# Kernel optimization log

Hardware: AMD Instinct MI355X
Metric: run time of the kernel (lower is better)

Reference implementation:

```python
import jax, jax.numpy as jnp
import numpy as np

BATCH, SEQ, HIDDEN = 2, 4096, 4096
HEADS, HEAD_DIM, BLOCK = 32, 128, 256
LAYER_IDX, N_LAYERS = 1, 32
EPS = 1e-5


def setup_inputs() -> dict:
    key = jax.random.key(0)
    ks = jax.random.split(key, 5)
    s = 0.02
    return {
        "hidden_states": jax.random.normal(ks[0], (BATCH, SEQ, HIDDEN), jnp.float32),
        "qkv_w": jax.random.normal(ks[1], (3 * HEADS * HEAD_DIM, HIDDEN), jnp.float32) * s,
        "out_w": jax.random.normal(ks[2], (HIDDEN, HEADS * HEAD_DIM), jnp.float32) * s,
        "gate_w": jax.random.normal(ks[3], (HEADS * HEAD_DIM, HIDDEN), jnp.float32) * s,
        "norm_w": jnp.ones((HEADS * HEAD_DIM,), jnp.float32),
    }


def _decays():
    # slope_rate: (h,1,1)
    base = 1.0 / 2.0 ** (8.0 / HEADS)
    exponent = jnp.arange(HEADS, dtype=jnp.float32) + 1.0
    factor = 1.0 - LAYER_IDX / (N_LAYERS - 1 + 1e-5) + 1e-5
    slope = (base ** exponent * factor)[:, None, None]
    r = jnp.arange(BLOCK, dtype=jnp.float32) + 1.0
    q_decay = jnp.exp(-slope * r[:, None])                 # (h, block, 1)
    k_decay = jnp.exp(-slope * (BLOCK - r)[:, None])       # (h, block, 1)
    diff = r[:, None] - r[None, :]                         # (block, block): i - j
    diag = slope[None] * diff[None, None]                  # (1, h, block, block)
    diag = jnp.where(diag >= 0, -diag, -jnp.inf)
    diag_decay = jnp.exp(diag)                             # causal intra-block decay
    block_decay = jnp.exp(-slope * BLOCK)                  # (h,1,1)
    return q_decay, k_decay, diag_decay, block_decay


def reference(hidden_states, qkv_w, out_w, gate_w, norm_w):
    b, s, _ = hidden_states.shape
    h, d, bs = HEADS, HEAD_DIM, BLOCK
    nb = s // bs
    q_decay, k_decay, diag_decay, block_decay = _decays()

    # qkv projection + silu, split per-head into q,k,v
    qkv = jax.nn.silu(hidden_states @ qkv_w.T)             # (b,s,3hd)
    qkv = qkv.reshape(b, s, h, 3, d)
    q = jnp.moveaxis(qkv[:, :, :, 0], 2, 1)                # (b,h,s,d)
    k = jnp.moveaxis(qkv[:, :, :, 1], 2, 1)
    v = jnp.moveaxis(qkv[:, :, :, 2], 2, 1)

    # split sequence into blocks, scan leading axis = block index
    def to_blocks(x):
        return jnp.moveaxis(x.reshape(b, h, nb, bs, d), 2, 0)  # (nb,b,h,bs,d)

    qb, kb, vb = to_blocks(q), to_blocks(k), to_blocks(v)

    def step(kv, blk):
        cq, ck, cv = blk
        # intra-block quadratic attention with causal decay
        scores = jnp.einsum('bhnd,bhmd->bhnm', cq, ck) * diag_decay
        intra = jnp.einsum('bhnm,bhmd->bhnd', scores, cv)
        # inter-block via decayed recurrent state kv: (b,h,d,d)
        inter = jnp.einsum('bhnd,bhde->bhne', cq * q_decay, kv)
        kv_next = kv * block_decay + jnp.einsum('bhnd,bhne->bhde', ck * k_decay, cv)
        return kv_next, intra + inter

    kv0 = jnp.zeros((b, h, d, d), hidden_states.dtype)
    _, out_blocks = jax.lax.scan(step, kv0, (qb, kb, vb))  # (nb,b,h,bs,d)

    attn = jnp.moveaxis(out_blocks, 0, 2)                  # (b,h,nb,bs,d)
    attn = attn.reshape(b, h, s, d).transpose(0, 2, 1, 3).reshape(b, s, h * d)

    # RMSNorm (fp32 accumulation, as MixtralRMSNorm)
    xf = attn.astype(jnp.float32)
    xf = xf * jax.lax.rsqrt(jnp.mean(xf * xf, axis=-1, keepdims=True) + EPS)
    normed = norm_w * xf.astype(attn.dtype)

    gate = jax.nn.sigmoid(hidden_states @ gate_w.T)
    return (gate * normed) @ out_w.T
```

## Files before the change

### kernel.cpp

```cpp
#include <hip/hip_runtime.h>

typedef unsigned short u16;
typedef __attribute__((ext_vector_type(4))) float f32x4;
typedef __attribute__((ext_vector_type(8))) __bf16 bf16x8;

#define SEQ   4096
#define HID   4096
#define HID3  12288

__device__ __forceinline__ float bf2f(u16 u){
  union { unsigned int i; float f; } v; v.i = ((unsigned int)u) << 16; return v.f;
}
__device__ __forceinline__ u16 f2bf(float f){
  union { float f; unsigned int i; } v; v.f = f;
  unsigned int r = (v.i + 0x7FFFu + ((v.i >> 16) & 1u)) >> 16;
  return (u16)r;
}
__device__ __forceinline__ float slope_of(int h){
  const float factor = 1.0f - 1.0f/(31.0f + 1e-5f) + 1e-5f;
  return exp2f(-0.25f * (float)(h + 1)) * factor;
}
__device__ __forceinline__ bf16x8 ld_bf8(const u16* p){
  return __builtin_bit_cast(bf16x8, *(const uint4*)p);
}
__device__ __forceinline__ void gload_lds16(const u16* g, u16* l){
  __builtin_amdgcn_global_load_lds((const __attribute__((address_space(1))) void*)g,
                                   (__attribute__((address_space(3))) void*)l, 16, 0, 0);
}

#define CVT_B0 33554432L
#define CVT_B1 83886080L
#define CVT_B2 100663296L
#define CVT_B3 117440512L
__global__ __launch_bounds__(256) void cvt4_kernel(const float* __restrict__ s0,
                                                   const float* __restrict__ s1,
                                                   const float* __restrict__ s2,
                                                   const float* __restrict__ s3,
                                                   u16* __restrict__ dst){
  long i = ((long)blockIdx.x * 256 + threadIdx.x) * 4;
  long stride = (long)gridDim.x * 1024;
  for (; i < CVT_B3; i += stride){
    const float* src;
    long off;
    if (i < CVT_B0){ src = s0; off = i; }
    else if (i < CVT_B1){ src = s1; off = i - CVT_B0; }
    else if (i < CVT_B2){ src = s2; off = i - CVT_B1; }
    else { src = s3; off = i - CVT_B2; }
    float4 v = *(const float4*)(src + off);
    ushort4 o;
    o.x = f2bf(v.x); o.y = f2bf(v.y); o.z = f2bf(v.z); o.w = f2bf(v.w);
    *(ushort4*)(dst + i) = o;
  }
}

template<int EPI>
__global__ __launch_bounds__(512) void gemm256(
    const u16* __restrict__ A, const u16* __restrict__ B, void* __restrict__ C,
    const u16* __restrict__ Aux, int M, int N, int K)
{
  __shared__ u16 ring[5][16384];
  const int t = threadIdx.x;
  const int w = t >> 6, l = t & 63, lr = l & 15, lk = l >> 4;
  const int mw = w >> 2, nw = w & 3;
  const int nbn = N >> 8;
  int nwg = gridDim.x;
  int bid = blockIdx.x;
  int bswz = (bid & 7) * (nwg >> 3) + (bid >> 3);
  int bm = bswz / nbn, bn = bswz % nbn;
  const u16* Abase = A + (long)(bm * 256) * K;
  const u16* Bbase = B + (long)(bn * 256) * K;
  const int NT = K >> 6;

  int sr[2], sku[2];
#pragma unroll
  for (int i = 0; i < 2; ++i){
    int dr = i * 64 + (t >> 3);
    int ul = (t & 7) ^ (dr & 7);
    sr[i]  = 2 * dr + (ul >> 2);
    sku[i] = ul & 3;
  }
  int offA[8], offB[4];
#pragma unroll
  for (int fn = 0; fn < 8; ++fn){
    int row = mw * 128 + fn * 16 + lr;
    offA[fn] = (row >> 1) * 64 + (((((row & 1) << 2) + lk) ^ ((row >> 1) & 7)) << 3);
  }
#pragma unroll
  for (int fe = 0; fe < 4; ++fe){
    int row = nw * 64 + fe * 16 + lr;
    offB[fe] = (row >> 1) * 64 + (((((row & 1) << 2) + lk) ^ ((row >> 1) & 7)) << 3);
  }

  auto stageA = [&](int kt, int c, int slot, int i){
    gload_lds16(Abase + (long)sr[i] * K + kt * 64 + c * 32 + sku[i] * 8,
                &ring[slot][i * 4096 + w * 512]);
  };
  auto stageB = [&](int kt, int c, int slot, int i){
    gload_lds16(Bbase + (long)sr[i] * K + kt * 64 + c * 32 + sku[i] * 8,
                &ring[slot][8192 + i * 4096 + w * 512]);
  };

  f32x4 acc[8][4] = {};

  stageA(0,0,0,0); stageA(0,0,0,1); stageB(0,0,0,0); stageB(0,0,0,1);
  stageA(0,1,1,0); stageA(0,1,1,1); stageB(0,1,1,0); stageB(0,1,1,1);
  if (1 < NT){ stageA(1,0,2,0); stageA(1,0,2,1); stageB(1,0,2,0); stageB(1,0,2,1); }
  asm volatile("s_waitcnt vmcnt(4)" ::: "memory");
  __builtin_amdgcn_s_barrier();

  int sa = 0;
  for (int p = 0; p < NT; ++p){
    int sb = sa + 1; if (sb >= 5) sb -= 5;
    int sx = sa + 3; if (sx >= 5) sx -= 5;
    int sy = sa + 4; if (sy >= 5) sy -= 5;
    const u16* Aa = &ring[sa][0];
    const u16* Ab = &ring[sb][0];
    const u16* Ba = &ring[sa][8192];
    const u16* Bb = &ring[sb][8192];
    bf16x8 bh0[4], bh1[4], afc0[8], afc1[8];

#pragma unroll
    for (int fe = 0; fe < 4; ++fe) bh0[fe] = ld_bf8(Ba + offB[fe]);
#pragma unroll
    for (int fn = 0; fn < 4; ++fn) afc0[fn] = ld_bf8(Aa + offA[fn]);
#pragma unroll
    for (int fn = 4; fn < 8; ++fn) afc0[fn] = ld_bf8(Aa + offA[fn]);
    if (p + 1 < NT){ stageA(p+1, 1, sx, 0); stageA(p+1, 1, sx, 1); }
    asm volatile("s_waitcnt lgkmcnt(4)" ::: "memory");
    __builtin_amdgcn_sched_barrier(0);
    __builtin_amdgcn_s_setprio(1);
#pragma unroll
    for (int fn = 0; fn < 4; ++fn)
#pragma unroll
      for (int fe = 0; fe < 4; ++fe)
        acc[fn][fe] = __builtin_amdgcn_mfma_f32_16x16x32_bf16(afc0[fn], bh0[fe], acc[fn][fe], 0, 0, 0);
    __builtin_amdgcn_s_setprio(0);

#pragma unroll
    for (int fe = 0; fe < 4; ++fe) bh1[fe] = ld_bf8(Bb + offB[fe]);
#pragma unroll
    for (int fn = 0; fn < 4; ++fn) afc1[fn] = ld_bf8(Ab + offA[fn]);
    if (p + 1 < NT){ stageB(p+1, 1, sx, 0); stageB(p+1, 1, sx, 1); }
    asm volatile("s_waitcnt lgkmcnt(8)" ::: "memory");
    __builtin_amdgcn_sched_barrier(0);
    __builtin_amdgcn_s_setprio(1);
#pragma unroll
    for (int fn = 4; fn < 8; ++fn)
#pragma unroll
      for (int fe = 0; fe < 4; ++fe)
        acc[fn][fe] = __builtin_amdgcn_mfma_f32_16x16x32_bf16(afc0[fn], bh0[fe], acc[fn][fe], 0, 0, 0);
    __builtin_amdgcn_s_setprio(0);

#pragma unroll
    for (int fn = 4; fn < 8; ++fn) afc1[fn] = ld_bf8(Ab + offA[fn]);
    if (p + 2 < NT){ stageA(p+2, 0, sy, 0); stageA(p+2, 0, sy, 1); }
    asm volatile("s_waitcnt lgkmcnt(4)" ::: "memory");
    __builtin_amdgcn_sched_barrier(0);
    __builtin_amdgcn_s_setprio(1);
#pragma unroll
    for (int fn = 0; fn < 4; ++fn)
#pragma unroll
      for (int fe = 0; fe < 4; ++fe)
        acc[fn][fe] = __builtin_amdgcn_mfma_f32_16x16x32_bf16(afc1[fn], bh1[fe], acc[fn][fe], 0, 0, 0);
    __builtin_amdgcn_s_setprio(0);

    if (p + 2 < NT){ stageB(p+2, 0, sy, 0); stageB(p+2, 0, sy, 1); }
    asm volatile("s_waitcnt lgkmcnt(0)" ::: "memory");
    __builtin_amdgcn_sched_barrier(0);
    __builtin_amdgcn_s_setprio(1);
#pragma unroll
    for (int fn = 4; fn < 8; ++fn)
#pragma unroll
      for (int fe = 0; fe < 4; ++fe)
        acc[fn][fe] = __builtin_amdgcn_mfma_f32_16x16x32_bf16(afc1[fn], bh1[fe], acc[fn][fe], 0, 0, 0);
    __builtin_amdgcn_s_setprio(0);

    if (p + 2 < NT) asm volatile("s_waitcnt vmcnt(4)" ::: "memory");
    else            asm volatile("s_waitcnt vmcnt(0)" ::: "memory");
    __builtin_amdgcn_s_barrier();
    sa += 2; if (sa >= 5) sa -= 5;
  }

  long crow = (long)bm * 256 + mw * 128 + lk * 4;
  long ccol = (long)bn * 256 + nw * 64 + lr;
#pragma unroll
  for (int fn = 0; fn < 8; ++fn)
#pragma unroll
    for (int fe = 0; fe < 4; ++fe)
#pragma unroll
      for (int reg = 0; reg < 4; ++reg){
        long row = crow + fn * 16 + reg;
        long col = ccol + fe * 16;
        float x = acc[fn][fe][reg];
        if (EPI == 0){
          ((u16*)C)[row * N + col] = f2bf(x / (1.0f + __expf(-x)));
        } else if (EPI == 1){
          float g = 1.0f / (1.0f + __expf(-x));
          ((u16*)C)[row * N + col] = f2bf(g * bf2f(Aux[row * N + col]));
        } else {
          ((float*)C)[row * N + col] = x;
        }
      }
}

__global__ __launch_bounds__(256) void attn_contrib(
    const u16* __restrict__ qkv, float* __restrict__ ct)
{
  __shared__ u16 VT[128 * 258];
  __shared__ u16 KT[128 * 258];
  int wg = blockIdx.x;
  int bh = wg >> 4, blk = wg & 15;
  int b = bh >> 5, h = bh & 31;
  int t = threadIdx.x;
  float slope = slope_of(h);
  const u16* kg = qkv + ((long)(b * SEQ + blk * 256)) * HID3 + h * 384 + 128;
  const u16* vg = kg + 128;
#pragma unroll
  for (int i = 0; i < 16; ++i){
    int chunk = t + i * 256;
    int row = chunk >> 4, c8 = (chunk & 15) << 3;
    float kd = __expf(-slope * (float)(255 - row));
    uint4 kk = *(const uint4*)&kg[(long)row * HID3 + c8];
    uint4 vv = *(const uint4*)&vg[(long)row * HID3 + c8];
    const u16* ks = (const u16*)&kk;
    const u16* vs = (const u16*)&vv;
#pragma unroll
    for (int x = 0; x < 8; ++x){
      KT[(c8 + x) * 258 + row] = f2bf(bf2f(ks[x]) * kd);
      VT[(c8 + x) * 258 + row] = vs[x];
    }
  }
  __syncthreads();
  int w = t >> 6, l = t & 63, lr = l & 15, lk = l >> 4;
  int we = (w >> 1) * 64, wd = (w & 1) * 64;
  f32x4 acc[4][4] = {};
  for (int nc = 0; nc < 8; ++nc){
    bf16x8 va[4], kb[4];
#pragma unroll
    for (int f = 0; f < 4; ++f) va[f] = ld_bf8(&VT[(we + f * 16 + lr) * 258 + nc * 32 + lk * 8]);
#pragma unroll
    for (int f = 0; f < 4; ++f) kb[f] = ld_bf8(&KT[(wd + f * 16 + lr) * 258 + nc * 32 + lk * 8]);
#pragma unroll
    for (int fe = 0; fe < 4; ++fe)
#pragma unroll
      for (int fd = 0; fd < 4; ++fd)
        acc[fe][fd] = __builtin_amdgcn_mfma_f32_16x16x32_bf16(va[fe], kb[fd], acc[fe][fd], 0, 0, 0);
  }
  float* out = ct + (long)wg * 16384;
#pragma unroll
  for (int fe = 0; fe < 4; ++fe)
#pragma unroll
    for (int fd = 0; fd < 4; ++fd)
#pragma unroll
      for (int reg = 0; reg < 4; ++reg){
        int e = we + fe * 16 + lk * 4 + reg;
        int d = wd + fd * 16 + lr;
        out[e * 128 + d] = acc[fe][fd][reg];
      }
}

__global__ __launch_bounds__(256) void attn_scan(const float* __restrict__ ct,
                                                 u16* __restrict__ stTb)
{
  int g = blockIdx.x;
  int bh = g >> 2, sl = g & 3;
  int t = threadIdx.x;
  float bdec = __expf(-slope_of(bh & 31) * 256.0f);
  float cur[16];
#pragma unroll
  for (int i = 0; i < 16; ++i) cur[i] = 0.f;
  const float* base = ct + (long)bh * 16 * 16384 + sl * 4096;
  u16* ob = stTb + (long)bh * 16 * 16384 + sl * 4096;
  for (int blkI = 0; blkI < 16; ++blkI){
    const float* p = base + (long)blkI * 16384;
    u16* o = ob + (long)blkI * 16384;
#pragma unroll
    for (int i = 0; i < 16; ++i){
      o[t + i * 256] = f2bf(cur[i]);
      cur[i] = cur[i] * bdec + p[t + i * 256];
    }
  }
}

__global__ __launch_bounds__(512) void attn_mfma(
    const u16* __restrict__ qkv, const u16* __restrict__ stTb, u16* __restrict__ attn)
{
  __shared__ u16 Ks[256 * 130];
  __shared__ u16 VTs[128 * 258];
  __shared__ u16 Ps[4][64 * 34];
  int wg = blockIdx.x;
  int bh = wg >> 4, blk = wg & 15;
  int b = bh >> 5, h = bh & 31;
  int t = threadIdx.x;
  int w = t >> 6, l = t & 63, lr = l & 15, lk = l >> 4;
  int r = w >> 1, c = w & 1;
  float slope = slope_of(h);
  const u16* qg = qkv + ((long)(b * SEQ + blk * 256)) * HID3 + h * 384;
  const u16* kg = qg + 128;
  const u16* vg = qg + 256;

#pragma unroll
  for (int i = 0; i < 8; ++i){
    int chunk = t + i * 512;
    int row = chunk >> 4, c8 = (chunk & 15) << 3;
    *(uint4*)&Ks[row * 130 + c8] = *(const uint4*)&kg[(long)row * HID3 + c8];
    uint4 vv = *(const uint4*)&vg[(long)row * HID3 + c8];
    const u16* vs = (const u16*)&vv;
#pragma unroll
    for (int x = 0; x < 8; ++x) VTs[(c8 + x) * 258 + row] = vs[x];
  }
  bf16x8 qa[4][4];
#pragma unroll
  for (int fn = 0; fn < 4; ++fn)
#pragma unroll
    for (int kc = 0; kc < 4; ++kc)
      qa[fn][kc] = ld_bf8(&qg[(long)(r * 64 + fn * 16 + lr) * HID3 + kc * 32 + lk * 8]);
  f32x4 acc[4][4] = {};
  __syncthreads();

  int mtmax = 2 * r + 1;
  for (int mt = 0; mt < 8; ++mt){
    if (mt <= mtmax){
      f32x4 S[4] = {};
      int mrow = mt * 32 + c * 16 + lr;
      bf16x8 kb[4];
#pragma unroll
      for (int kc = 0; kc < 4; ++kc)
        kb[kc] = ld_bf8(&Ks[mrow * 130 + kc * 32 + lk * 8]);
#pragma unroll
      for (int fn = 0; fn < 4; ++fn)
#pragma unroll
        for (int kc = 0; kc < 4; ++kc)
          S[fn] = __builtin_amdgcn_mfma_f32_16x16x32_bf16(qa[fn][kc], kb[kc], S[fn], 0, 0, 0);
      int m = mt * 32 + c * 16 + lr;
#pragma unroll
      for (int fn = 0; fn < 4; ++fn)
#pragma unroll
        for (int reg = 0; reg < 4; ++reg){
          int n = r * 64 + fn * 16 + lk * 4 + reg;
          float dv = (n >= m) ? __expf(-slope * (float)(n - m)) : 0.f;
          Ps[r][(fn * 16 + lk * 4 + reg) * 34 + c * 16 + lr] = f2bf(S[fn][reg] * dv);
        }
    }
    __syncthreads();
    if (mt <= mtmax){
      bf16x8 pa[4], vb[4];
#pragma unroll
      for (int fn = 0; fn < 4; ++fn)
        pa[fn] = ld_bf8(&Ps[r][(fn * 16 + lr) * 34 + lk * 8]);
#pragma unroll
      for (int fe = 0; fe < 4; ++fe)
        vb[fe] = ld_bf8(&VTs[(c * 64 + fe * 16 + lr) * 258 + mt * 32 + lk * 8]);
#pragma unroll
      for (int fn = 0; fn < 4; ++fn)
#pragma unroll
        for (int fe = 0; fe < 4; ++fe)
          acc[fn][fe] = __builtin_amdgcn_mfma_f32_16x16x32_bf16(pa[fn], vb[fe], acc[fn][fe], 0, 0, 0);
    }
    __syncthreads();
  }

#pragma unroll
  for (int fn = 0; fn < 4; ++fn){
    int n = r * 64 + fn * 16 + lr;
    float qd = __expf(-slope * (float)(n + 1));
#pragma unroll
    for (int kc = 0; kc < 4; ++kc){
      union { bf16x8 v; u16 u[8]; } uu; uu.v = qa[fn][kc];
#pragma unroll
      for (int x = 0; x < 8; ++x) uu.u[x] = f2bf(bf2f(uu.u[x]) * qd);
      qa[fn][kc] = uu.v;
    }
  }
  const u16* sg = stTb + (long)(bh * 16 + blk) * 16384;
#pragma unroll
  for (int kc = 0; kc < 4; ++kc){
    bf16x8 sb2[4];
#pragma unroll
    for (int fe = 0; fe < 4; ++fe)
      sb2[fe] = ld_bf8(&sg[(c * 64 + fe * 16 + lr) * 128 + kc * 32 + lk * 8]);
#pragma unroll
    for (int fn = 0; fn < 4; ++fn)
#pragma unroll
      for (int fe = 0; fe < 4; ++fe)
        acc[fn][fe] = __builtin_amdgcn_mfma_f32_16x16x32_bf16(qa[fn][kc], sb2[fe], acc[fn][fe], 0, 0, 0);
  }

  u16* arow = attn + ((long)(b * SEQ + blk * 256)) * HID + h * 128;
#pragma unroll
  for (int fn = 0; fn < 4; ++fn)
#pragma unroll
    for (int fe = 0; fe < 4; ++fe)
#pragma unroll
      for (int reg = 0; reg < 4; ++reg){
        int n = r * 64 + fn * 16 + lk * 4 + reg;
        int col = c * 64 + fe * 16 + lr;
        arow[(long)n * HID + col] = f2bf(acc[fn][fe][reg]);
      }
}

__global__ __launch_bounds__(256) void rmsnorm_ip(u16* __restrict__ attn,
                                                  const float* __restrict__ nw)
{
  __shared__ float wsum[4];
  int row = blockIdx.x, t = threadIdx.x;
  u16* p = attn + (long)row * HID;
  uint4 v0 = *(const uint4*)&p[t * 8];
  uint4 v1 = *(const uint4*)&p[t * 8 + 2048];
  const u16* a0 = (const u16*)&v0;
  const u16* a1 = (const u16*)&v1;
  float f0[8], f1[8];
  float ss = 0.f;
#pragma unroll
  for (int x = 0; x < 8; ++x){
    f0[x] = bf2f(a0[x]); f1[x] = bf2f(a1[x]);
    ss += f0[x] * f0[x] + f1[x] * f1[x];
  }
#pragma unroll
  for (int off = 32; off > 0; off >>= 1) ss += __shfl_down(ss, off);
  if ((t & 63) == 0) wsum[t >> 6] = ss;
  __syncthreads();
  float rs = rsqrtf((wsum[0] + wsum[1] + wsum[2] + wsum[3]) * (1.0f / 4096.0f) + 1e-5f);
  alignas(16) u16 o0[8], o1[8];
#pragma unroll
  for (int x = 0; x < 8; ++x){
    o0[x] = f2bf(f0[x] * rs * nw[t * 8 + x]);
    o1[x] = f2bf(f1[x] * rs * nw[t * 8 + 2048 + x]);
  }
  *(uint4*)&p[t * 8]        = *(const uint4*)&o0[0];
  *(uint4*)&p[t * 8 + 2048] = *(const uint4*)&o1[0];
}

extern "C" void kernel_launch(void* const* d_in, const int* in_sizes, int n_in,
                              void* d_out, int out_size, void* d_ws, size_t ws_size,
                              hipStream_t stream)
{
  const float* hidden = (const float*)d_in[0];
  const float* qkv_w  = (const float*)d_in[1];
  const float* out_w  = (const float*)d_in[2];
  const float* gate_w = (const float*)d_in[3];
  const float* norm_w = (const float*)d_in[4];
  char* ws = (char*)d_ws;
  const long SZ_X  = 67108864L;
  const long SZ_WQ = 100663296L;
  const long SZ_WG = 33554432L;
  const long SZ_WO = 33554432L;
  const long SZ_QA = 201326592L;
  const long SZ_AT = 67108864L;
  u16* Xb   = (u16*)(ws);
  u16* Wq   = (u16*)(ws + SZ_X);
  u16* Wg   = (u16*)(ws + SZ_X + SZ_WQ);
  u16* Wo   = (u16*)(ws + SZ_X + SZ_WQ + SZ_WG);
  u16* qact = (u16*)(ws + SZ_X + SZ_WQ + SZ_WG + SZ_WO);
  u16* attn = (u16*)(ws + SZ_X + SZ_WQ + SZ_WG + SZ_WO + SZ_QA);
  float* st   = (float*)Wq;
  u16*   stTb = (u16*)(ws + SZ_X + 67108864L);
  u16* gated = qact;
  if (ws_size < (size_t)(SZ_X + SZ_WQ + SZ_WG + SZ_WO + SZ_QA + SZ_AT)) return;

  cvt4_kernel<<<2048, 256, 0, stream>>>(hidden, qkv_w, gate_w, out_w, Xb);

  gemm256<0><<<32 * 48, 512, 0, stream>>>(Xb, Wq, (void*)qact, nullptr, 8192, 12288, 4096);

  attn_contrib<<<1024, 256, 0, stream>>>(qact, st);
  attn_scan<<<256, 256, 0, stream>>>(st, stTb);
  attn_mfma<<<1024, 512, 0, stream>>>(qact, stTb, attn);
  rmsnorm_ip<<<8192, 256, 0, stream>>>(attn, norm_w);

  gemm256<1><<<32 * 16, 512, 0, stream>>>(Xb, Wg, (void*)gated, attn, 8192, 4096, 4096);
  gemm256<2><<<32 * 16, 512, 0, stream>>>(gated, Wo, d_out, nullptr, 8192, 4096, 4096);
}
```

Baseline: 1.590 ms.

## Use 4-wave 256x256 GEMM tiles with 128x128 per-wave subtiles

Changes the GEMM workgroup from 8 waves (each computing 128x64) to 4 waves (each computing 128x128), doubling per-wave register accumulators and fragment reuse. The staging loops now issue four global-to-LDS loads per stage per thread, and the vmcnt/lgkmcnt waits are adjusted to match. This raises the MFMA-to-LDS-read ratio and cuts the LDS traffic per FLOP. The cost is heavy VGPR/AGPR pressure (64 accumulator tiles), fewer waves to hide latency, and a possible risk of register spills.

```diff
diff --git a/kernel.cpp b/kernel.cpp
--- a/kernel.cpp
+++ b/kernel.cpp
@@ -54,14 +54,14 @@
 }
 
 template<int EPI>
-__global__ __launch_bounds__(512) void gemm256(
+__global__ __launch_bounds__(256, 1) void gemm256(
     const u16* __restrict__ A, const u16* __restrict__ B, void* __restrict__ C,
     const u16* __restrict__ Aux, int M, int N, int K)
 {
   __shared__ u16 ring[5][16384];
   const int t = threadIdx.x;
   const int w = t >> 6, l = t & 63, lr = l & 15, lk = l >> 4;
-  const int mw = w >> 2, nw = w & 3;
+  const int mw = w >> 1, nw = w & 1;
   const int nbn = N >> 8;
   int nwg = gridDim.x;
   int bid = blockIdx.x;
@@ -71,41 +71,45 @@
   const u16* Bbase = B + (long)(bn * 256) * K;
   const int NT = K >> 6;
 
-  int sr[2], sku[2];
-#pragma unroll
-  for (int i = 0; i < 2; ++i){
-    int dr = i * 64 + (t >> 3);
+  int sr[4], sku[4];
+#pragma unroll
+  for (int i = 0; i < 4; ++i){
+    int dr = i * 32 + (t >> 3);
     int ul = (t & 7) ^ (dr & 7);
     sr[i]  = 2 * dr + (ul >> 2);
     sku[i] = ul & 3;
   }
-  int offA[8], offB[4];
+  int offA[8], offB[8];
 #pragma unroll
   for (int fn = 0; fn < 8; ++fn){
     int row = mw * 128 + fn * 16 + lr;
     offA[fn] = (row >> 1) * 64 + (((((row & 1) << 2) + lk) ^ ((row >> 1) & 7)) << 3);
   }
 #pragma unroll
-  for (int fe = 0; fe < 4; ++fe){
-    int row = nw * 64 + fe * 16 + lr;
+  for (int fe = 0; fe < 8; ++fe){
+    int row = nw * 128 + fe * 16 + lr;
     offB[fe] = (row >> 1) * 64 + (((((row & 1) << 2) + lk) ^ ((row >> 1) & 7)) << 3);
   }
 
-  auto stageA = [&](int kt, int c, int slot, int i){
-    gload_lds16(Abase + (long)sr[i] * K + kt * 64 + c * 32 + sku[i] * 8,
-                &ring[slot][i * 4096 + w * 512]);
+  auto stageA = [&](int kt, int c, int slot){
+#pragma unroll
+    for (int i = 0; i < 4; ++i)
+      gload_lds16(Abase + (long)sr[i] * K + kt * 64 + c * 32 + sku[i] * 8,
+                  &ring[slot][i * 2048 + w * 512]);
   };
-  auto stageB = [&](int kt, int c, int slot, int i){
-    gload_lds16(Bbase + (long)sr[i] * K + kt * 64 + c * 32 + sku[i] * 8,
-                &ring[slot][8192 + i * 4096 + w * 512]);
+  auto stageB = [&](int kt, int c, int slot){
+#pragma unroll
+    for (int i = 0; i < 4; ++i)
+      gload_lds16(Bbase + (long)sr[i] * K + kt * 64 + c * 32 + sku[i] * 8,
+                  &ring[slot][8192 + i * 2048 + w * 512]);
   };
 
-  f32x4 acc[8][4] = {};
-
-  stageA(0,0,0,0); stageA(0,0,0,1); stageB(0,0,0,0); stageB(0,0,0,1);
-  stageA(0,1,1,0); stageA(0,1,1,1); stageB(0,1,1,0); stageB(0,1,1,1);
-  if (1 < NT){ stageA(1,0,2,0); stageA(1,0,2,1); stageB(1,0,2,0); stageB(1,0,2,1); }
-  asm volatile("s_waitcnt vmcnt(4)" ::: "memory");
+  f32x4 acc[8][8] = {};
+
+  stageA(0,0,0); stageB(0,0,0);
+  stageA(0,1,1); stageB(0,1,1);
+  if (1 < NT){ stageA(1,0,2); stageB(1,0,2); }
+  asm volatile("s_waitcnt vmcnt(8)" ::: "memory");
   __builtin_amdgcn_s_barrier();
 
   int sa = 0;
@@ -117,76 +121,76 @@
     const u16* Ab = &ring[sb][0];
     const u16* Ba = &ring[sa][8192];
     const u16* Bb = &ring[sb][8192];
-    bf16x8 bh0[4], bh1[4], afc0[8], afc1[8];
-
-#pragma unroll
-    for (int fe = 0; fe < 4; ++fe) bh0[fe] = ld_bf8(Ba + offB[fe]);
-#pragma unroll
-    for (int fn = 0; fn < 4; ++fn) afc0[fn] = ld_bf8(Aa + offA[fn]);
-#pragma unroll
-    for (int fn = 4; fn < 8; ++fn) afc0[fn] = ld_bf8(Aa + offA[fn]);
-    if (p + 1 < NT){ stageA(p+1, 1, sx, 0); stageA(p+1, 1, sx, 1); }
+    bf16x8 a0[8], b0[8], a1[8], b1[8];
+
+#pragma unroll
+    for (int fn = 0; fn < 4; ++fn) a0[fn] = ld_bf8(Aa + offA[fn]);
+#pragma unroll
+    for (int fe = 0; fe < 8; ++fe) b0[fe] = ld_bf8(Ba + offB[fe]);
+#pragma unroll
+    for (int fn = 4; fn < 8; ++fn) a0[fn] = ld_bf8(Aa + offA[fn]);
+    if (p + 1 < NT) stageA(p+1, 1, sx);
     asm volatile("s_waitcnt lgkmcnt(4)" ::: "memory");
     __builtin_amdgcn_sched_barrier(0);
     __builtin_amdgcn_s_setprio(1);
 #pragma unroll
     for (int fn = 0; fn < 4; ++fn)
 #pragma unroll
-      for (int fe = 0; fe < 4; ++fe)
-        acc[fn][fe] = __builtin_amdgcn_mfma_f32_16x16x32_bf16(afc0[fn], bh0[fe], acc[fn][fe], 0, 0, 0);
+      for (int fe = 0; fe < 8; ++fe)
+        acc[fn][fe] = __builtin_amdgcn_mfma_f32_16x16x32_bf16(a0[fn], b0[fe], acc[fn][fe], 0, 0, 0);
     __builtin_amdgcn_s_setprio(0);
 
 #pragma unroll
-    for (int fe = 0; fe < 4; ++fe) bh1[fe] = ld_bf8(Bb + offB[fe]);
-#pragma unroll
-    for (int fn = 0; fn < 4; ++fn) afc1[fn] = ld_bf8(Ab + offA[fn]);
-    if (p + 1 < NT){ stageB(p+1, 1, sx, 0); stageB(p+1, 1, sx, 1); }
-    asm volatile("s_waitcnt lgkmcnt(8)" ::: "memory");
+    for (int fn = 0; fn < 4; ++fn) a1[fn] = ld_bf8(Ab + offA[fn]);
+#pragma unroll
+    for (int fe = 0; fe < 8; ++fe) b1[fe] = ld_bf8(Bb + offB[fe]);
+    if (p + 1 < NT) stageB(p+1, 1, sx);
+    asm volatile("s_waitcnt lgkmcnt(12)" ::: "memory");
     __builtin_amdgcn_sched_barrier(0);
     __builtin_amdgcn_s_setprio(1);
 #pragma unroll
     for (int fn = 4; fn < 8; ++fn)
 #pragma unroll
-      for (int fe = 0; fe < 4; ++fe)
-        acc[fn][fe] = __builtin_amdgcn_mfma_f32_16x16x32_bf16(afc0[fn], bh0[fe], acc[fn][fe], 0, 0, 0);
+      for (int fe = 0; fe < 8; ++fe)
+        acc[fn][fe] = __builtin_amdgcn_mfma_f32_16x16x32_bf16(a0[fn], b0[fe], acc[fn][fe], 0, 0, 0);
     __builtin_amdgcn_s_setprio(0);
 
 #pragma unroll
-    for (int fn = 4; fn < 8; ++fn) afc1[fn] = ld_bf8(Ab + offA[fn]);
-    if (p + 2 < NT){ stageA(p+2, 0, sy, 0); stageA(p+2, 0, sy, 1); }
+    for (int fn = 4; fn < 8; ++fn) a1[fn] = ld_bf8(Ab + offA[fn]);
+    if (p + 2 < NT) stageA(p+2, 0, sy);
     asm volatile("s_waitcnt lgkmcnt(4)" ::: "memory");
     __builtin_amdgcn_sched_barrier(0);
     __builtin_amdgcn_s_setprio(1);
 #pragma unroll
     for (int fn = 0; fn < 4; ++fn)
 #pragma unroll
-      for (int fe = 0; fe < 4; ++fe)
-        acc[fn][fe] = __builtin_amdgcn_mfma_f32_16x16x32_bf16(afc1[fn], bh1[fe], acc[fn][fe], 0, 0, 0);
+      for (int fe = 0; fe < 8; ++fe)
+        acc[fn][fe] = __builtin_amdgcn_mfma_f32_16x16x32_bf16(a1[fn], b1[fe], acc[fn][fe], 0, 0, 0);
     __builtin_amdgcn_s_setprio(0);
 
-    if (p + 2 < NT){ stageB(p+2, 0, sy, 0); stageB(p+2, 0, sy, 1); }
+    if (p + 2 < NT) stageB(p+2, 0, sy);
     asm volatile("s_waitcnt lgkmcnt(0)" ::: "memory");
     __builtin_amdgcn_sched_barrier(0);
     __builtin_amdgcn_s_setprio(1);
 #pragma unroll
     for (int fn = 4; fn < 8; ++fn)
 #pragma unroll
-      for (int fe = 0; fe < 4; ++fe)
-        acc[fn][fe] = __builtin_amdgcn_mfma_f32_16x16x32_bf16(afc1[fn], bh1[fe], acc[fn][fe], 0, 0, 0);
+      for (int fe = 0; fe < 8; ++fe)
+        acc[fn][fe] = __builtin_amdgcn_mfma_f32_16x16x32_bf16(a1[fn], b1[fe], acc[fn][fe], 0, 0, 0);
     __builtin_amdgcn_s_setprio(0);
 
-    if (p + 2 < NT) asm volatile("s_waitcnt vmcnt(4)" ::: "memory");
+    if (p + 2 < NT) asm volatile("s_waitcnt vmcnt(8)" ::: "memory");
     else            asm volatile("s_waitcnt vmcnt(0)" ::: "memory");
     __builtin_amdgcn_s_barrier();
     sa += 2; if (sa >= 5) sa -= 5;
   }
 
   long crow = (long)bm * 256 + mw * 128 + lk * 4;
-  long ccol = (long)bn * 256 + nw * 64 + lr;
+  long ccol = (long)bn * 256 + nw * 128 + lr;
 #pragma unroll
   for (int fn = 0; fn < 8; ++fn)
 #pragma unroll
-    for (int fe = 0; fe < 4; ++fe)
+    for (int fe = 0; fe < 8; ++fe)
 #pragma unroll
       for (int reg = 0; reg < 4; ++reg){
         long row = crow + fn * 16 + reg;
@@ -460,13 +464,13 @@
 
   cvt4_kernel<<<2048, 256, 0, stream>>>(hidden, qkv_w, gate_w, out_w, Xb);
 
-  gemm256<0><<<32 * 48, 512, 0, stream>>>(Xb, Wq, (void*)qact, nullptr, 8192, 12288, 4096);
+  gemm256<0><<<32 * 48, 256, 0, stream>>>(Xb, Wq, (void*)qact, nullptr, 8192, 12288, 4096);
 
   attn_contrib<<<1024, 256, 0, stream>>>(qact, st);
   attn_scan<<<256, 256, 0, stream>>>(st, stTb);
   attn_mfma<<<1024, 512, 0, stream>>>(qact, stTb, attn);
   rmsnorm_ip<<<8192, 256, 0, stream>>>(attn, norm_w);
 
-  gemm256<1><<<32 * 16, 512, 0, stream>>>(Xb, Wg, (void*)gated, attn, 8192, 4096, 4096);
-  gemm256<2><<<32 * 16, 512, 0, stream>>>(gated, Wo, d_out, nullptr, 8192, 4096, 4096);
-}
+  gemm256<1><<<32 * 16, 256, 0, stream>>>(Xb, Wg, (void*)gated, attn, 8192, 4096, 4096);
+  gemm256<2><<<32 * 16, 256, 0, stream>>>(gated, Wo, d_out, nullptr, 8192, 4096, 4096);
+}
```

New measurement: 1.965 ms. +23.6%, slower.
